# Performance work log

Hardware: AMD Instinct MI355X
Metric: run time of the kernel (lower is better)

Reference implementation:

```python
import jax, jax.numpy as jnp
import numpy as np

B, T, IN, E, D, O = 32, 256, 64, 128, 128, 32


def _lstm_scan(x_tbi, Wih, Whh, b, h0, c0):
    # x_tbi: [T,B,in]; returns hidden states [T,B,H]; PyTorch gate order i,f,g,o
    def step(carry, xt):
        h, c = carry
        z = xt @ Wih.T + h @ Whh.T + b
        i, f, g, o = jnp.split(z, 4, axis=-1)
        c = jax.nn.sigmoid(f) * c + jax.nn.sigmoid(i) * jnp.tanh(g)
        h = jax.nn.sigmoid(o) * jnp.tanh(c)
        return (h, c), h
    _, hs = jax.lax.scan(step, (h0, c0), x_tbi)
    return hs


def setup_inputs() -> dict:
    key = jax.random.key(0)
    ks = jax.random.split(key, 20)
    def u(k, shape, fan):
        s = 1.0 / np.sqrt(fan)
        return jax.random.uniform(k, shape, jnp.float32, -s, s)
    x = jax.random.normal(ks[0], (B, T, IN), jnp.float32)
    lengths = jnp.sort(jax.random.randint(ks[1], (B,), T // 2, T + 1))[::-1]
    lengths = lengths.at[0].set(T)  # pad_packed max length == T
    return {
        "x": x,
        "input_lengths": lengths,
        "dec_h0": jax.random.normal(ks[2], (B, D), jnp.float32),
        "dec_c0": jax.random.normal(ks[3], (B, D), jnp.float32),
        "Wih_f": u(ks[4], (4 * E, IN), E), "Whh_f": u(ks[5], (4 * E, E), E), "b_f": u(ks[6], (4 * E,), E),
        "Wih_b": u(ks[7], (4 * E, IN), E), "Whh_b": u(ks[8], (4 * E, E), E), "b_b": u(ks[9], (4 * E,), E),
        "Wa": u(ks[10], (D, D + 2 * E), D + 2 * E), "ba": u(ks[11], (D,), D + 2 * E),
        "v": jax.random.uniform(ks[12], (D,), jnp.float32, 0.0, 1.0),
        "Wih_d": u(ks[13], (4 * D, 2 * E + O), D), "Whh_d": u(ks[14], (4 * D, D), D), "b_d": u(ks[15], (4 * D,), D),
        "Wl": u(ks[16], (O, 2 * E + D), 2 * E + D), "bl": u(ks[17], (O,), 2 * E + D),
    }


def _forward(x, input_lengths, dec_h0, dec_c0, Wih_f, Whh_f, b_f, Wih_b, Whh_b, b_b,
             Wa, ba, v, Wih_d, Whh_d, b_d, Wl, bl):
    mask = jnp.arange(T)[None, :] < input_lengths[:, None]  # [B,T] valid positions
    z0 = jnp.zeros((B, E), x.dtype)
    # --- bidirectional encoder (packed-sequence semantics) ---
    hf = _lstm_scan(x.transpose(1, 0, 2), Wih_f, Whh_f, b_f, z0, z0).transpose(1, 0, 2)  # [B,T,E]
    # backward dir: reverse each valid span, scan, reverse back
    rev_idx = jnp.where(mask, input_lengths[:, None] - 1 - jnp.arange(T)[None, :], 0)  # [B,T]
    xr = jnp.take_along_axis(x, rev_idx[:, :, None], axis=1)
    hb_r = _lstm_scan(xr.transpose(1, 0, 2), Wih_b, Whh_b, b_b, z0, z0).transpose(1, 0, 2)
    hb = jnp.take_along_axis(hb_r, rev_idx[:, :, None], axis=1)
    enc = jnp.concatenate([hf, hb], -1) * mask[:, :, None]  # [B,T,2E], zeros past length
    # --- decoder with additive attention ---
    Wa_h, Wa_e = Wa[:, :D], Wa[:, D:]
    enc_proj = enc @ Wa_e.T + ba  # [B,T,D], constant across decoder steps
    def dec_step(carry, _):
        hidden, y = carry
        e = jnp.tanh(enc_proj + (hidden @ Wa_h.T)[:, None, :])  # [B,T,D]
        s = jnp.where(mask, e @ v, -jnp.inf)                     # length-masked scores
        a = jax.nn.softmax(s, axis=1)
        ctx = jnp.einsum('bt,bte->be', a, enc)                   # [B,2E]
        di = jnp.concatenate([y, ctx], -1)                       # [B,O+2E]
        # NOTE: original resets the decoder LSTM to (dec_h0, dec_c0) every step
        z = di @ Wih_d.T + dec_h0 @ Whh_d.T + b_d
        i, f, g, o = jnp.split(z, 4, axis=-1)
        c = jax.nn.sigmoid(f) * dec_c0 + jax.nn.sigmoid(i) * jnp.tanh(g)
        h = jax.nn.sigmoid(o) * jnp.tanh(c)
        y_new = jnp.concatenate([h, ctx], -1) @ Wl.T + bl        # [B,O]
        return (h, y_new), y_new
    y0 = jnp.zeros((B, O), x.dtype)
    _, ys = jax.lax.scan(dec_step, (dec_h0, y0), None, length=T)  # [T,B,O]
    out = ys.transpose(1, 0, 2).reshape(B, T * O)
    # original prepends a zeros[B,O] block then slices [:, 1:]
    out = jnp.concatenate([jnp.zeros((B, O), x.dtype), out], axis=1)
    return out[:, 1:]


def reference(x, input_lengths, dec_h0, dec_c0, Wih_f, Whh_f, b_f, Wih_b, Whh_b, b_b,
              Wa, ba, v, Wih_d, Whh_d, b_d, Wl, bl):
    return _forward(x, input_lengths, dec_h0, dec_c0, Wih_f, Whh_f, b_f, Wih_b, Whh_b, b_b,
                    Wa, ba, v, Wih_d, Whh_d, b_d, Wl, bl)
```

## Files before the change

kernel.cpp:

```cpp
#include <hip/hip_runtime.h>

#define BB 32
#define TT 256
#define INP 64
#define EE 128
#define DD 128
#define OO 32

#define OFF_XWF    0u
#define OFF_ENCWH  0u
#define OFF_XWB    4194304u
#define OFF_EPT    4194304u
#define OFF_ENCWLH 5242880u
#define OFF_HF     8388608u
#define OFF_HBR    9437184u
#define OFF_ZC     10485760u
#define OFF_WHHTF  10502144u
#define OFF_WHHTB  10567680u
#define OFF_WIHTF  10633216u
#define OFF_WIHTB  10665984u
#define OFF_WHHDT  10698752u
#define OFF_WCAT   10764288u
#define OFF_WLHT   10936320u
#define OFF_WAHH   10940416u
#define OFF_WYH    10948608u

typedef _Float16 h2_t __attribute__((ext_vector_type(2)));

__device__ __forceinline__ float fexp2(float x){ return __builtin_amdgcn_exp2f(x); }
__device__ __forceinline__ float frcp(float x){ return __builtin_amdgcn_rcpf(x); }
__device__ __forceinline__ float fsig(float x){ return frcp(1.0f + fexp2(-1.4426950408889634f * x)); }
__device__ __forceinline__ float ftanh_(float x){ return 1.0f - 2.0f * frcp(1.0f + fexp2(2.8853900817779268f * x)); }
__device__ __forceinline__ float packh2(float a, float b){
  h2_t t; t.x = (_Float16)a; t.y = (_Float16)b; return __builtin_bit_cast(float, t);
}
__device__ __forceinline__ h2_t ash2(float f){ return __builtin_bit_cast(h2_t, f); }
__device__ __forceinline__ float fdot2_(float a, float b, float c){
  return __builtin_amdgcn_fdot2(ash2(a), ash2(b), c, false);
}

#define C2F 2.8853900817779268f
#define L2E 1.4426950408889634f

__global__ void pack_kernel(const float* __restrict__ Whh_f, const float* __restrict__ Whh_b,
                            const float* __restrict__ Wih_f, const float* __restrict__ Wih_b,
                            const float* __restrict__ Whh_d, const float* __restrict__ Wa,
                            const float* __restrict__ Wih_d, const float* __restrict__ Wl,
                            float* __restrict__ ws){
  unsigned e = blockIdx.x * 256u + threadIdx.x;
  if (e < 65536u){ unsigned j=e>>7, k=e&127u; ws[OFF_WHHTF + (k>>2)*2048u + j*4u + (k&3u)] = Whh_f[e]; return; }
  e -= 65536u;
  if (e < 65536u){ unsigned j=e>>7, k=e&127u; ws[OFF_WHHTB + (k>>2)*2048u + j*4u + (k&3u)] = Whh_b[e]; return; }
  e -= 65536u;
  if (e < 32768u){ unsigned j=e>>6, i=e&63u; ws[OFF_WIHTF + (i>>2)*2048u + j*4u + (i&3u)] = Wih_f[e]; return; }
  e -= 32768u;
  if (e < 32768u){ unsigned j=e>>6, i=e&63u; ws[OFF_WIHTB + (i>>2)*2048u + j*4u + (i&3u)] = Wih_b[e]; return; }
  e -= 32768u;
  if (e < 65536u){ unsigned j=e>>7, k=e&127u; ws[OFF_WHHDT + (k>>2)*2048u + j*4u + (k&3u)] = Whh_d[e]; return; }
  e -= 65536u;
  if (e < 172032u){
    unsigned j = e >> 8, k = e & 255u;
    float val;
    if (j < 128u)      val = Wa[j*384u + 128u + k];
    else if (j < 640u) val = Wih_d[(j-128u)*288u + 32u + k];
    else               val = Wl[(j-640u)*384u + 128u + k];
    ws[OFF_WCAT + (k>>2)*2688u + j*4u + (k&3u)] = val; return;
  }
  e -= 172032u;
  if (e < 4096u){ unsigned k=e>>5, m=e&31u; ws[OFF_WLHT + (k>>2)*128u + m*4u + (k&3u)] = Wl[m*384u + k]; return; }
  e -= 4096u;
  if (e < 8192u){
    unsigned d = e >> 6, k2 = e & 63u;
    ws[OFF_WAHH + e] = packh2(Wa[d*384u + 2u*k2], Wa[d*384u + 2u*k2 + 1u]); return;
  }
  e -= 8192u;
  if (e < 8192u){
    unsigned m2 = e >> 9, j = e & 511u;
    ws[OFF_WYH + e] = packh2(Wih_d[j*288u + 2u*m2], Wih_d[j*288u + 2u*m2 + 1u]); return;
  }
}

__global__ __launch_bounds__(512) void zc_kernel(const float* __restrict__ dec_h0,
                                                 const float* __restrict__ b_d,
                                                 float* __restrict__ ws){
  __shared__ __align__(16) float h0[128];
  int b = blockIdx.x, j = threadIdx.x;
  if (j < 128) h0[j] = dec_h0[b*128 + j];
  __syncthreads();
  const float* WT = ws + OFF_WHHDT;
  float4 a4 = make_float4(0.f,0.f,0.f,0.f);
  #pragma unroll
  for (int k4 = 0; k4 < 32; k4++){
    float4 wv = *(const float4*)(WT + k4*2048 + j*4);
    float4 hv = *(const float4*)(h0 + k4*4);
    a4.x += wv.x*hv.x; a4.y += wv.y*hv.y; a4.z += wv.z*hv.z; a4.w += wv.w*hv.w;
  }
  ws[OFF_ZC + b*512 + j] = b_d[j] + (a4.x + a4.y) + (a4.z + a4.w);
}

__global__ __launch_bounds__(512) void xw_kernel(const float* __restrict__ x,
                                                 const int* __restrict__ lengths,
                                                 const float* __restrict__ b_f,
                                                 const float* __restrict__ b_b,
                                                 float* __restrict__ ws){
  int bx = blockIdx.x;
  int dir = bx >> 9, b = (bx >> 4) & 31, tile = bx & 15;
  int t0 = tile * 16;
  int len = lengths[b];
  __shared__ __align__(16) float xrow[16][64];
  const float* WT   = ws + (dir ? OFF_WIHTB : OFF_WIHTF);
  const float* bias = dir ? b_b : b_f;
  float* out = ws + (dir ? OFF_XWB : OFF_XWF) + (unsigned)b * TT * 512;
  int tid = threadIdx.x;
  for (int idx = tid; idx < 1024; idx += 512){
    int r = idx >> 6, i = idx & 63;
    int s = t0 + r;
    int src = dir ? ((s < len) ? (len - 1 - s) : 0) : s;
    xrow[r][i] = x[((unsigned)b * TT + src) * 64 + i];
  }
  __syncthreads();
  int j = tid;
  float bj = bias[j];
  float acc[16];
  #pragma unroll
  for (int r = 0; r < 16; r++) acc[r] = bj;
  #pragma unroll 4
  for (int i4 = 0; i4 < 16; i4++){
    float4 wv = *(const float4*)(WT + i4*2048 + j*4);
    #pragma unroll
    for (int r = 0; r < 16; r++){
      float4 xv = *(const float4*)(&xrow[r][i4*4]);
      acc[r] += wv.x*xv.x + wv.y*xv.y + wv.z*xv.z + wv.w*xv.w;
    }
  }
  #pragma unroll
  for (int r = 0; r < 16; r++) out[(t0 + r)*512 + j] = acc[r];
}

__global__ __launch_bounds__(512, 2) void lstm_kernel(const int* __restrict__ lengths,
                                                      float* __restrict__ ws){
  int bx = blockIdx.x;
  int b = bx & 31, dir = bx >> 5;
  int len = lengths[b];
  if (len < 1) len = 1; if (len > TT) len = TT;
  const float* xW = ws + (dir ? OFF_XWB : OFF_XWF) + (unsigned)b * TT * 512;
  const float* WT = ws + (dir ? OFF_WHHTB : OFF_WHHTF);
  float* hout = ws + (dir ? OFF_HBR : OFF_HF) + (unsigned)b * TT * 128;
  __shared__ __align__(16) float hsh[128];
  __shared__ __align__(16) float csh[128];
  __shared__ __align__(16) float zsh[512];
  int j = threadIdx.x;
  float w[128];
  #pragma unroll
  for (int k4 = 0; k4 < 32; k4++){
    float4 wv = *(const float4*)(WT + k4*2048 + j*4);
    w[k4*4+0] = wv.x; w[k4*4+1] = wv.y; w[k4*4+2] = wv.z; w[k4*4+3] = wv.w;
  }
  if (j < 128){ hsh[j] = 0.f; csh[j] = 0.f; }
  for (int t = 0; t < len; t++){
    __syncthreads();
    float4 a4 = make_float4(xW[t*512 + j], 0.f, 0.f, 0.f);
    #pragma unroll
    for (int k4 = 0; k4 < 32; k4++){
      float4 hv = *(const float4*)(hsh + k4*4);
      a4.x += w[k4*4+0]*hv.x; a4.y += w[k4*4+1]*hv.y;
      a4.z += w[k4*4+2]*hv.z; a4.w += w[k4*4+3]*hv.w;
    }
    zsh[j] = (a4.x + a4.y) + (a4.z + a4.w);
    __syncthreads();
    if (j < 128){
      float zi = zsh[j], zf = zsh[128+j], zg = zsh[256+j], zo = zsh[384+j];
      float c = fsig(zf)*csh[j] + fsig(zi)*ftanh_(zg);
      float h = fsig(zo)*ftanh_(c);
      csh[j] = c; hsh[j] = h;
      hout[t*128 + j] = h;
    }
  }
}

__global__ __launch_bounds__(192) void proj_kernel(const int* __restrict__ lengths,
                                                   const float* __restrict__ ba,
                                                   float* __restrict__ ws){
  int bx = blockIdx.x;
  int b = bx >> 4, tile = bx & 15;
  int len = lengths[b];
  if (len < 1) len = 1; if (len > TT) len = TT;
  int t0 = tile * 16;
  __shared__ __align__(16) float enc[16][256];
  int tid = threadIdx.x;
  const float* hf  = ws + OFF_HF  + (unsigned)b * TT * 128;
  const float* hbr = ws + OFF_HBR + (unsigned)b * TT * 128;
  for (int idx = tid; idx < 4096; idx += 192){
    int r = idx >> 8, k = idx & 255;
    int t = t0 + r;
    float vv = 0.f;
    if (t < len) vv = (k < 128) ? hf[t*128 + k] : hbr[(len-1-t)*128 + (k-128)];
    enc[r][k] = vv;
  }
  __syncthreads();
  if (tid >= 168) return;
  int j0 = tid * 4;
  float acc[16][4];
  #pragma unroll
  for (int r = 0; r < 16; r++){ acc[r][0]=0.f; acc[r][1]=0.f; acc[r][2]=0.f; acc[r][3]=0.f; }
  const float* WC = ws + OFF_WCAT;
  for (int k4 = 0; k4 < 64; k4++){
    float4 w0 = *(const float4*)(WC + k4*2688 + (j0+0)*4);
    float4 w1 = *(const float4*)(WC + k4*2688 + (j0+1)*4);
    float4 w2 = *(const float4*)(WC + k4*2688 + (j0+2)*4);
    float4 w3 = *(const float4*)(WC + k4*2688 + (j0+3)*4);
    #pragma unroll
    for (int r = 0; r < 16; r++){
      float4 ev = *(const float4*)(&enc[r][k4*4]);
      acc[r][0] += w0.x*ev.x + w0.y*ev.y + w0.z*ev.z + w0.w*ev.w;
      acc[r][1] += w1.x*ev.x + w1.y*ev.y + w1.z*ev.z + w1.w*ev.w;
      acc[r][2] += w2.x*ev.x + w2.y*ev.y + w2.z*ev.z + w2.w*ev.w;
      acc[r][3] += w3.x*ev.x + w3.y*ev.y + w3.z*ev.z + w3.w*ev.w;
    }
  }
  float* epo  = ws + OFF_EPT    + (unsigned)b * TT * 128;
  float* eWh  = ws + OFF_ENCWH  + (unsigned)b * 128 * 512;
  float* eWlh = ws + OFF_ENCWLH + (unsigned)b * 128 * 32;
  #pragma unroll
  for (int c = 0; c < 4; c++){
    int j = j0 + c;
    if (j < 128){
      float bj = ba[j];
      for (int r = 0; r < 16; r++) epo[(t0 + r)*128 + j] = (acc[r][c] + bj) * C2F;
    } else if (j < 640){
      for (int r2 = 0; r2 < 8; r2++)
        eWh[(tile*8 + r2)*512 + (j - 128)] = packh2(acc[2*r2][c], acc[2*r2+1][c]);
    } else {
      for (int r2 = 0; r2 < 8; r2++)
        eWlh[(tile*8 + r2)*32 + (j - 640)] = packh2(acc[2*r2][c], acc[2*r2+1][c]);
    }
  }
}

__global__ __launch_bounds__(512, 2) void decoder_kernel(const int* __restrict__ lengths,
                                                         const float* __restrict__ dec_h0,
                                                         const float* __restrict__ dec_c0,
                                                         const float* __restrict__ v,
                                                         const float* __restrict__ bl,
                                                         float* __restrict__ ws,
                                                         float* __restrict__ out){
  __shared__ __align__(16) float ep_lds[32768];
  __shared__ __align__(16) float red512[512];
  __shared__ __align__(16) float zsh[512];
  __shared__ __align__(16) float vqsh[256];
  __shared__ __align__(16) float hsh[128];
  __shared__ __align__(16) float c0sh[128];
  __shared__ __align__(16) float a_h2[128];
  __shared__ __align__(16) float h_h2[64];
  __shared__ __align__(16) float ylds[32];
  __shared__ __align__(16) float y_h2[16];
  __shared__ float redbuf[2], redbuf2[2], vsumsh;

  int b = blockIdx.x;
  int len = lengths[b];
  if (len < 1) len = 1; if (len > TT) len = TT;
  int tid = threadIdx.x;

  const float* EPT  = ws + OFF_EPT    + (unsigned)b * 32768;
  const float* EWH  = ws + OFF_ENCWH  + (unsigned)b * 65536;
  const float* EWLH = ws + OFF_ENCWLH + (unsigned)b * 4096;
  const float* WLHT = ws + OFF_WLHT;
  float* outp = out + (unsigned)b * 8223;

  float wreg[128];
  #pragma unroll
  for (int r = 0; r < 128; r++) wreg[r] = EWH[r*512 + tid];
  int d_ = tid & 127, p_ = tid >> 7;
  float wah[16];
  #pragma unroll
  for (int i = 0; i < 16; i++) wah[i] = ws[OFF_WAHH + d_*64 + p_*16 + i];
  float wy[16];
  #pragma unroll
  for (int i = 0; i < 16; i++) wy[i] = ws[OFF_WYH + i*512 + tid];
  float zc_r = ws[OFF_ZC + b*512 + tid];

  for (int c = 0; c < 64; c++){
    int idx = c*512 + tid;
    int t = idx >> 7, dd = idx & 127;
    ep_lds[t*128 + ((dd + 4*t) & 127)] = EPT[idx];
  }
  if (tid < 128){
    hsh[tid]  = dec_h0[b*128 + tid];
    c0sh[tid] = dec_c0[b*128 + tid];
    vqsh[2*tid+1] = v[tid];
  }
  if (tid < 64) h_h2[tid] = packh2(dec_h0[b*128 + 2*tid], dec_h0[b*128 + 2*tid + 1]);
  if (tid < 32) ylds[tid] = 0.f;
  if (tid < 16) y_h2[tid] = 0.f;
  if (tid < 31) outp[tid] = 0.f;
  if (tid == 0){ float s = 0.f; for (int k = 0; k < 128; k++) s += v[k]; vsumsh = s; }

  for (int t = 0; t < TT; t++){
    __syncthreads();
    if (tid < 16) y_h2[tid] = packh2(ylds[2*tid], ylds[2*tid+1]);
    {
      float qa = 0.f, qb = 0.f;
      #pragma unroll
      for (int i = 0; i < 16; i += 2){
        qa = fdot2_(h_h2[p_*16 + i],     wah[i],     qa);
        qb = fdot2_(h_h2[p_*16 + i + 1], wah[i + 1], qb);
      }
      red512[tid] = qa + qb;
    }
    __syncthreads();
    if (tid < 128)
      vqsh[2*tid] = (red512[tid] + red512[128+tid] + red512[256+tid] + red512[384+tid]) * C2F;
    __syncthreads();
    {
      int tt = tid & 255, half = tid >> 8;
      float4 P4 = make_float4(0.f,0.f,0.f,0.f);
      if (tt < len){
        const float* epr = ep_lds + tt*128;
        int rot = 4*tt;
        #pragma unroll 4
        for (int g = 0; g < 16; g++){
          int d0 = (half*16 + g)*4;
          float4 e4 = *(const float4*)(epr + ((d0 + rot) & 127));
          float4 vq0 = *(const float4*)(vqsh + 2*d0);
          float4 vq1 = *(const float4*)(vqsh + 2*d0 + 4);
          P4.x = fmaf(vq0.y, frcp(1.f + fexp2(e4.x + vq0.x)), P4.x);
          P4.y = fmaf(vq0.w, frcp(1.f + fexp2(e4.y + vq0.z)), P4.y);
          P4.z = fmaf(vq1.y, frcp(1.f + fexp2(e4.z + vq1.x)), P4.z);
          P4.w = fmaf(vq1.w, frcp(1.f + fexp2(e4.w + vq1.z)), P4.w);
        }
      }
      red512[tid] = (P4.x + P4.y) + (P4.z + P4.w);
    }
    __syncthreads();
    float s0 = -1e30f, s1 = -1e30f, e0 = 0.f, e1 = 0.f;
    if (tid < 128){
      int ta = 2*tid;
      if (ta < len)     s0 = vsumsh - 2.f*(red512[ta]   + red512[256+ta]);
      if (ta + 1 < len) s1 = vsumsh - 2.f*(red512[ta+1] + red512[256+ta+1]);
    }
    {
      float mm = fmaxf(s0, s1);
      #pragma unroll
      for (int off = 32; off; off >>= 1) mm = fmaxf(mm, __shfl_xor(mm, off));
      if (tid < 128 && (tid & 63) == 0) redbuf[tid>>6] = mm;
    }
    __syncthreads();
    if (tid < 128){
      float gm = fmaxf(redbuf[0], redbuf[1]);
      if (2*tid < len)     e0 = fexp2((s0 - gm) * L2E);
      if (2*tid + 1 < len) e1 = fexp2((s1 - gm) * L2E);
    }
    {
      float ss = e0 + e1;
      #pragma unroll
      for (int off = 32; off; off >>= 1) ss += __shfl_xor(ss, off);
      if (tid < 128 && (tid & 63) == 0) redbuf2[tid>>6] = ss;
    }
    __syncthreads();
    if (tid < 128){
      float rl = frcp(redbuf2[0] + redbuf2[1]);
      a_h2[tid] = packh2(e0 * rl, e1 * rl);
    }
    __syncthreads();
    {
      float za = 0.f, zb = 0.f, zc2 = 0.f, zd = 0.f;
      #pragma unroll
      for (int r4 = 0; r4 < 32; r4++){
        za  = fdot2_(a_h2[4*r4+0], wreg[4*r4+0], za);
        zb  = fdot2_(a_h2[4*r4+1], wreg[4*r4+1], zb);
        zc2 = fdot2_(a_h2[4*r4+2], wreg[4*r4+2], zc2);
        zd  = fdot2_(a_h2[4*r4+3], wreg[4*r4+3], zd);
      }
      #pragma unroll
      for (int i4 = 0; i4 < 4; i4++){
        za  = fdot2_(y_h2[4*i4+0], wy[4*i4+0], za);
        zb  = fdot2_(y_h2[4*i4+1], wy[4*i4+1], zb);
        zc2 = fdot2_(y_h2[4*i4+2], wy[4*i4+2], zc2);
        zd  = fdot2_(y_h2[4*i4+3], wy[4*i4+3], zd);
      }
      zsh[tid] = zc_r + ((za + zb) + (zc2 + zd));
    }
    __syncthreads();
    if (tid < 128){
      float zi = zsh[tid], zf = zsh[128+tid], zg = zsh[256+tid], zo = zsh[384+tid];
      float c = fsig(zf)*c0sh[tid] + fsig(zi)*ftanh_(zg);
      hsh[tid] = fsig(zo)*ftanh_(c);
    }
    __syncthreads();
    if (tid >= 256 && tid < 320){
      int i = tid - 256;
      h_h2[i] = packh2(hsh[2*i], hsh[2*i+1]);
    }
    if (tid < 256){
      int m = tid & 31, p = tid >> 5;
      float acc = 0.f;
      #pragma unroll
      for (int ri = 0; ri < 16; ri++){
        int r = p + ri*8;
        acc = fdot2_(a_h2[r], EWLH[r*32 + m], acc);
      }
      #pragma unroll
      for (int k4 = p; k4 < 32; k4 += 8){
        float4 hv = *(const float4*)(hsh + k4*4);
        float4 wv = *(const float4*)(WLHT + k4*128 + m*4);
        acc += hv.x*wv.x + hv.y*wv.y + hv.z*wv.z + hv.w*wv.w;
      }
      red512[tid] = acc;
    }
    __syncthreads();
    if (tid < 32){
      float y = bl[tid];
      #pragma unroll
      for (int p2 = 0; p2 < 8; p2++) y += red512[p2*32 + tid];
      ylds[tid] = y;
      outp[31 + t*32 + tid] = y;
    }
  }
}

extern "C" void kernel_launch(void* const* d_in, const int* in_sizes, int n_in,
                              void* d_out, int out_size, void* d_ws, size_t ws_size,
                              hipStream_t stream){
  const float* x       = (const float*)d_in[0];
  const int*   lengths = (const int*)  d_in[1];
  const float* dec_h0  = (const float*)d_in[2];
  const float* dec_c0  = (const float*)d_in[3];
  const float* Wih_f   = (const float*)d_in[4];
  const float* Whh_f   = (const float*)d_in[5];
  const float* b_f     = (const float*)d_in[6];
  const float* Wih_b   = (const float*)d_in[7];
  const float* Whh_b   = (const float*)d_in[8];
  const float* b_b     = (const float*)d_in[9];
  const float* Wa      = (const float*)d_in[10];
  const float* ba      = (const float*)d_in[11];
  const float* v       = (const float*)d_in[12];
  const float* Wih_d   = (const float*)d_in[13];
  const float* Whh_d   = (const float*)d_in[14];
  const float* b_d     = (const float*)d_in[15];
  const float* Wl      = (const float*)d_in[16];
  const float* bl      = (const float*)d_in[17];
  float* ws  = (float*)d_ws;
  float* out = (float*)d_out;

  pack_kernel<<<1776, 256, 0, stream>>>(Whh_f, Whh_b, Wih_f, Wih_b, Whh_d, Wa, Wih_d, Wl, ws);
  zc_kernel<<<32, 512, 0, stream>>>(dec_h0, b_d, ws);
  xw_kernel<<<1024, 512, 0, stream>>>(x, lengths, b_f, b_b, ws);
  lstm_kernel<<<64, 512, 0, stream>>>(lengths, ws);
  proj_kernel<<<512, 192, 0, stream>>>(lengths, ba, ws);
  decoder_kernel<<<32, 512, 0, stream>>>(lengths, dec_h0, dec_c0, v, bl, ws, out);
}
```

Measured before the change: 1.984 ms.

## Use MFMA for decoder gate and query matvecs, restructure attention reduction

Replaces the per-thread fdot2 loops for the attention query projection and the decoder gate pre-activation with 16x16x32 f16 MFMA instructions, holding the weight fragments in registers as half8 vectors. The attention score pass is reorganised so each thread handles 16 timesteps times 4 feature columns, with a shuffle plus a rotated LDS pool reduction. The softmax is merged into a single pass that combines per-wave max and sum, which removes several barriers per step. This trades the simpler layout for MFMA fragment bookkeeping and broadcasts one batch row across the MFMA M dimension, so most of each matrix op's rows are wasted work.

Result: slower. 2.919 ms (+47.1%).

```diff
diff --git a/kernel.cpp b/kernel.cpp
--- a/kernel.cpp
+++ b/kernel.cpp
@@ -26,6 +26,8 @@
 #define OFF_WYH    10948608u
 
 typedef _Float16 h2_t __attribute__((ext_vector_type(2)));
+typedef _Float16 half8_t __attribute__((ext_vector_type(8)));
+typedef float f32x4_t __attribute__((ext_vector_type(4)));
 
 __device__ __forceinline__ float fexp2(float x){ return __builtin_amdgcn_exp2f(x); }
 __device__ __forceinline__ float frcp(float x){ return __builtin_amdgcn_rcpf(x); }
@@ -245,21 +247,22 @@
                                                          float* __restrict__ ws,
                                                          float* __restrict__ out){
   __shared__ __align__(16) float ep_lds[32768];
-  __shared__ __align__(16) float red512[512];
-  __shared__ __align__(16) float zsh[512];
-  __shared__ __align__(16) float vqsh[256];
+  __shared__ __align__(16) float pool[4096];
+  __shared__ __align__(16) float qsh[128];
+  __shared__ __align__(16) float au_h2[144];
   __shared__ __align__(16) float hsh[128];
   __shared__ __align__(16) float c0sh[128];
-  __shared__ __align__(16) float a_h2[128];
   __shared__ __align__(16) float h_h2[64];
   __shared__ __align__(16) float ylds[32];
-  __shared__ __align__(16) float y_h2[16];
-  __shared__ float redbuf[2], redbuf2[2], vsumsh;
+  __shared__ float mlsw[8];
 
   int b = blockIdx.x;
   int len = lengths[b];
   if (len < 1) len = 1; if (len > TT) len = TT;
   int tid = threadIdx.x;
+  int lane = tid & 63, w = tid >> 6;
+  int rg = lane >> 4, c16 = lane & 15;
+  int dg = tid & 31, tg = tid >> 5;
 
   const float* EPT  = ws + OFF_EPT    + (unsigned)b * 32768;
   const float* EWH  = ws + OFF_ENCWH  + (unsigned)b * 65536;
@@ -267,122 +270,148 @@
   const float* WLHT = ws + OFF_WLHT;
   float* outp = out + (unsigned)b * 8223;
 
-  float wreg[128];
-  #pragma unroll
-  for (int r = 0; r < 128; r++) wreg[r] = EWH[r*512 + tid];
-  int d_ = tid & 127, p_ = tid >> 7;
-  float wah[16];
-  #pragma unroll
-  for (int i = 0; i < 16; i++) wah[i] = ws[OFF_WAHH + d_*64 + p_*16 + i];
-  float wy[16];
-  #pragma unroll
-  for (int i = 0; i < 16; i++) wy[i] = ws[OFF_WYH + i*512 + tid];
-  float zc_r = ws[OFF_ZC + b*512 + tid];
-
-  for (int c = 0; c < 64; c++){
-    int idx = c*512 + tid;
-    int t = idx >> 7, dd = idx & 127;
-    ep_lds[t*128 + ((dd + 4*t) & 127)] = EPT[idx];
+  half8_t bfr[4][9];
+  #pragma unroll
+  for (int nt = 0; nt < 4; nt++){
+    int j = w*64 + nt*16 + c16;
+    #pragma unroll
+    for (int ks = 0; ks < 8; ks++){
+      float4 tmp;
+      tmp.x = EWH[(ks*16 + rg*4 + 0)*512 + j];
+      tmp.y = EWH[(ks*16 + rg*4 + 1)*512 + j];
+      tmp.z = EWH[(ks*16 + rg*4 + 2)*512 + j];
+      tmp.w = EWH[(ks*16 + rg*4 + 3)*512 + j];
+      bfr[nt][ks] = __builtin_bit_cast(half8_t, tmp);
+    }
+    {
+      float4 tmp;
+      tmp.x = ws[OFF_WYH + (rg*4 + 0)*512 + j];
+      tmp.y = ws[OFF_WYH + (rg*4 + 1)*512 + j];
+      tmp.z = ws[OFF_WYH + (rg*4 + 2)*512 + j];
+      tmp.w = ws[OFF_WYH + (rg*4 + 3)*512 + j];
+      bfr[nt][8] = __builtin_bit_cast(half8_t, tmp);
+    }
+  }
+  half8_t wab[4];
+  {
+    int dq = w*16 + c16;
+    #pragma unroll
+    for (int ks = 0; ks < 4; ks++){
+      float4 tmp;
+      tmp.x = ws[OFF_WAHH + dq*64 + ks*16 + rg*4 + 0];
+      tmp.y = ws[OFF_WAHH + dq*64 + ks*16 + rg*4 + 1];
+      tmp.z = ws[OFF_WAHH + dq*64 + ks*16 + rg*4 + 2];
+      tmp.w = ws[OFF_WAHH + dq*64 + ks*16 + rg*4 + 3];
+      wab[ks] = __builtin_bit_cast(half8_t, tmp);
+    }
+  }
+  float zcs[4];
+  #pragma unroll
+  for (int nt = 0; nt < 4; nt++) zcs[nt] = ws[OFF_ZC + b*512 + w*64 + nt*16 + c16];
+  float4 vreg;
+  vreg.x = v[4*dg + 0]; vreg.y = v[4*dg + 1]; vreg.z = v[4*dg + 2]; vreg.w = v[4*dg + 3];
+
+  {
+    const float4* src = (const float4*)EPT;
+    float4* dst = (float4*)ep_lds;
+    #pragma unroll
+    for (int c = 0; c < 16; c++) dst[c*512 + tid] = src[c*512 + tid];
   }
   if (tid < 128){
     hsh[tid]  = dec_h0[b*128 + tid];
     c0sh[tid] = dec_c0[b*128 + tid];
-    vqsh[2*tid+1] = v[tid];
   }
   if (tid < 64) h_h2[tid] = packh2(dec_h0[b*128 + 2*tid], dec_h0[b*128 + 2*tid + 1]);
   if (tid < 32) ylds[tid] = 0.f;
-  if (tid < 16) y_h2[tid] = 0.f;
   if (tid < 31) outp[tid] = 0.f;
-  if (tid == 0){ float s = 0.f; for (int k = 0; k < 128; k++) s += v[k]; vsumsh = s; }
 
   for (int t = 0; t < TT; t++){
     __syncthreads();
-    if (tid < 16) y_h2[tid] = packh2(ylds[2*tid], ylds[2*tid+1]);
+    if (tid < 16) au_h2[128 + tid] = packh2(ylds[2*tid], ylds[2*tid+1]);
     {
-      float qa = 0.f, qb = 0.f;
-      #pragma unroll
-      for (int i = 0; i < 16; i += 2){
-        qa = fdot2_(h_h2[p_*16 + i],     wah[i],     qa);
-        qb = fdot2_(h_h2[p_*16 + i + 1], wah[i + 1], qb);
-      }
-      red512[tid] = qa + qb;
-    }
-    __syncthreads();
-    if (tid < 128)
-      vqsh[2*tid] = (red512[tid] + red512[128+tid] + red512[256+tid] + red512[384+tid]) * C2F;
+      f32x4_t qa = {0.f, 0.f, 0.f, 0.f};
+      #pragma unroll
+      for (int ks = 0; ks < 4; ks++){
+        float4 hf4 = *(const float4*)(h_h2 + ks*16 + rg*4);
+        qa = __builtin_amdgcn_mfma_f32_16x16x32_f16(__builtin_bit_cast(half8_t, hf4), wab[ks], qa, 0, 0, 0);
+      }
+      if (rg == 0) qsh[w*16 + c16] = qa[0] * C2F;
+    }
     __syncthreads();
     {
-      int tt = tid & 255, half = tid >> 8;
-      float4 P4 = make_float4(0.f,0.f,0.f,0.f);
-      if (tt < len){
-        const float* epr = ep_lds + tt*128;
-        int rot = 4*tt;
-        #pragma unroll 4
-        for (int g = 0; g < 16; g++){
-          int d0 = (half*16 + g)*4;
-          float4 e4 = *(const float4*)(epr + ((d0 + rot) & 127));
-          float4 vq0 = *(const float4*)(vqsh + 2*d0);
-          float4 vq1 = *(const float4*)(vqsh + 2*d0 + 4);
-          P4.x = fmaf(vq0.y, frcp(1.f + fexp2(e4.x + vq0.x)), P4.x);
-          P4.y = fmaf(vq0.w, frcp(1.f + fexp2(e4.y + vq0.z)), P4.y);
-          P4.z = fmaf(vq1.y, frcp(1.f + fexp2(e4.z + vq1.x)), P4.z);
-          P4.w = fmaf(vq1.w, frcp(1.f + fexp2(e4.w + vq1.z)), P4.w);
+      float4 q4 = *(const float4*)(qsh + 4*dg);
+      float p[16];
+      int t0 = tg * 16;
+      #pragma unroll
+      for (int k = 0; k < 16; k++){
+        float pk = 0.f;
+        if (t0 + k < len){
+          float4 e4 = *(const float4*)(ep_lds + (t0 + k)*128 + 4*dg);
+          pk  =      vreg.x * frcp(1.f + fexp2(e4.x + q4.x));
+          pk = fmaf(vreg.y, frcp(1.f + fexp2(e4.y + q4.y)), pk);
+          pk = fmaf(vreg.z, frcp(1.f + fexp2(e4.z + q4.z)), pk);
+          pk = fmaf(vreg.w, frcp(1.f + fexp2(e4.w + q4.w)), pk);
         }
-      }
-      red512[tid] = (P4.x + P4.y) + (P4.z + P4.w);
-    }
-    __syncthreads();
-    float s0 = -1e30f, s1 = -1e30f, e0 = 0.f, e1 = 0.f;
+        p[k] = pk;
+      }
+      #pragma unroll
+      for (int k = 0; k < 16; k++) p[k] += __shfl_xor(p[k], 16);
+      if (dg < 16){
+        #pragma unroll
+        for (int k = 0; k < 16; k++)
+          pool[dg*256 + ((t0 + k + dg) & 255)] = p[k];
+      }
+    }
+    __syncthreads();
+    float e = 0.f, mm = -1e30f;
+    if (tid < 256){
+      float s = -1e30f;
+      if (tid < len){
+        float ps = 0.f;
+        #pragma unroll
+        for (int dgi = 0; dgi < 16; dgi++)
+          ps += pool[dgi*256 + ((tid + dgi) & 255)];
+        s = ps * (-2.f * L2E);
+      }
+      mm = s;
+      #pragma unroll
+      for (int off = 32; off; off >>= 1) mm = fmaxf(mm, __shfl_xor(mm, off));
+      if (tid < len) e = fexp2(s - mm);
+      float ss = e;
+      #pragma unroll
+      for (int off = 32; off; off >>= 1) ss += __shfl_xor(ss, off);
+      if ((tid & 63) == 0){ mlsw[(tid>>6)*2] = mm; mlsw[(tid>>6)*2 + 1] = ss; }
+    }
+    __syncthreads();
+    if (tid < 256){
+      float gm = fmaxf(fmaxf(mlsw[0], mlsw[2]), fmaxf(mlsw[4], mlsw[6]));
+      float tot = mlsw[1]*fexp2(mlsw[0] - gm) + mlsw[3]*fexp2(mlsw[2] - gm)
+                + mlsw[5]*fexp2(mlsw[4] - gm) + mlsw[7]*fexp2(mlsw[6] - gm);
+      float scale = fexp2(mm - gm) * frcp(tot);
+      float e1 = __shfl_xor(e, 1);
+      if (!(tid & 1)) au_h2[tid >> 1] = packh2(e*scale, e1*scale);
+    }
+    __syncthreads();
+    {
+      f32x4_t a0 = {zcs[0], zcs[0], zcs[0], zcs[0]};
+      f32x4_t a1 = {zcs[1], zcs[1], zcs[1], zcs[1]};
+      f32x4_t a2 = {zcs[2], zcs[2], zcs[2], zcs[2]};
+      f32x4_t a3 = {zcs[3], zcs[3], zcs[3], zcs[3]};
+      #pragma unroll
+      for (int ks = 0; ks < 9; ks++){
+        float4 af = *(const float4*)(au_h2 + ks*16 + rg*4);
+        half8_t a8 = __builtin_bit_cast(half8_t, af);
+        a0 = __builtin_amdgcn_mfma_f32_16x16x32_f16(a8, bfr[0][ks], a0, 0, 0, 0);
+        a1 = __builtin_amdgcn_mfma_f32_16x16x32_f16(a8, bfr[1][ks], a1, 0, 0, 0);
+        a2 = __builtin_amdgcn_mfma_f32_16x16x32_f16(a8, bfr[2][ks], a2, 0, 0, 0);
+        a3 = __builtin_amdgcn_mfma_f32_16x16x32_f16(a8, bfr[3][ks], a3, 0, 0, 0);
+      }
+      float zv = (rg == 0) ? a0[0] : (rg == 1) ? a1[0] : (rg == 2) ? a2[0] : a3[0];
+      pool[tid] = zv;
+    }
+    __syncthreads();
     if (tid < 128){
-      int ta = 2*tid;
-      if (ta < len)     s0 = vsumsh - 2.f*(red512[ta]   + red512[256+ta]);
-      if (ta + 1 < len) s1 = vsumsh - 2.f*(red512[ta+1] + red512[256+ta+1]);
-    }
-    {
-      float mm = fmaxf(s0, s1);
-      #pragma unroll
-      for (int off = 32; off; off >>= 1) mm = fmaxf(mm, __shfl_xor(mm, off));
-      if (tid < 128 && (tid & 63) == 0) redbuf[tid>>6] = mm;
-    }
-    __syncthreads();
-    if (tid < 128){
-      float gm = fmaxf(redbuf[0], redbuf[1]);
-      if (2*tid < len)     e0 = fexp2((s0 - gm) * L2E);
-      if (2*tid + 1 < len) e1 = fexp2((s1 - gm) * L2E);
-    }
-    {
-      float ss = e0 + e1;
-      #pragma unroll
-      for (int off = 32; off; off >>= 1) ss += __shfl_xor(ss, off);
-      if (tid < 128 && (tid & 63) == 0) redbuf2[tid>>6] = ss;
-    }
-    __syncthreads();
-    if (tid < 128){
-      float rl = frcp(redbuf2[0] + redbuf2[1]);
-      a_h2[tid] = packh2(e0 * rl, e1 * rl);
-    }
-    __syncthreads();
-    {
-      float za = 0.f, zb = 0.f, zc2 = 0.f, zd = 0.f;
-      #pragma unroll
-      for (int r4 = 0; r4 < 32; r4++){
-        za  = fdot2_(a_h2[4*r4+0], wreg[4*r4+0], za);
-        zb  = fdot2_(a_h2[4*r4+1], wreg[4*r4+1], zb);
-        zc2 = fdot2_(a_h2[4*r4+2], wreg[4*r4+2], zc2);
-        zd  = fdot2_(a_h2[4*r4+3], wreg[4*r4+3], zd);
-      }
-      #pragma unroll
-      for (int i4 = 0; i4 < 4; i4++){
-        za  = fdot2_(y_h2[4*i4+0], wy[4*i4+0], za);
-        zb  = fdot2_(y_h2[4*i4+1], wy[4*i4+1], zb);
-        zc2 = fdot2_(y_h2[4*i4+2], wy[4*i4+2], zc2);
-        zd  = fdot2_(y_h2[4*i4+3], wy[4*i4+3], zd);
-      }
-      zsh[tid] = zc_r + ((za + zb) + (zc2 + zd));
-    }
-    __syncthreads();
-    if (tid < 128){
-      float zi = zsh[tid], zf = zsh[128+tid], zg = zsh[256+tid], zo = zsh[384+tid];
+      float zi = pool[tid], zf = pool[128+tid], zg = pool[256+tid], zo = pool[384+tid];
       float c = fsig(zf)*c0sh[tid] + fsig(zi)*ftanh_(zg);
       hsh[tid] = fsig(zo)*ftanh_(c);
     }
@@ -392,26 +421,26 @@
       h_h2[i] = packh2(hsh[2*i], hsh[2*i+1]);
     }
     if (tid < 256){
-      int m = tid & 31, p = tid >> 5;
+      int m = tid & 31, pp = tid >> 5;
       float acc = 0.f;
       #pragma unroll
       for (int ri = 0; ri < 16; ri++){
-        int r = p + ri*8;
-        acc = fdot2_(a_h2[r], EWLH[r*32 + m], acc);
-      }
-      #pragma unroll
-      for (int k4 = p; k4 < 32; k4 += 8){
+        int r = pp + ri*8;
+        acc = fdot2_(au_h2[r], EWLH[r*32 + m], acc);
+      }
+      #pragma unroll
+      for (int k4 = pp; k4 < 32; k4 += 8){
         float4 hv = *(const float4*)(hsh + k4*4);
         float4 wv = *(const float4*)(WLHT + k4*128 + m*4);
         acc += hv.x*wv.x + hv.y*wv.y + hv.z*wv.z + hv.w*wv.w;
       }
-      red512[tid] = acc;
+      pool[tid] = acc;
     }
     __syncthreads();
     if (tid < 32){
       float y = bl[tid];
       #pragma unroll
-      for (int p2 = 0; p2 < 8; p2++) y += red512[p2*32 + tid];
+      for (int p2 = 0; p2 < 8; p2++) y += pool[p2*32 + tid];
       ylds[tid] = y;
       outp[31 + t*32 + tid] = y;
     }
```
